# Optimization experiments

Hardware: AMD Instinct MI355X
Metric: run time of the kernel (lower is better)

The kernel has to match this reference:

```python
import jax, jax.numpy as jnp
import numpy as np

B, L, D, H = 2, 1024, 1024, 16
HEAD = D // H
BUCKETS = 256
MAX_REL = 512
ATT_SPAN = BUCKETS          # pos_ebd_size = position_buckets when buckets > 0
SCALE_FACTOR = 3            # 1 (content) + 1 (c2p) + 1 (p2c)


def _log_bucket(rel, bucket_size, max_position):
    """make_log_bucket_position: signed log-bucketed relative positions."""
    sign = jnp.sign(rel).astype(jnp.float32)
    mid = bucket_size // 2
    abs_pos = jnp.where((rel < mid) & (rel > -mid), mid - 1, jnp.abs(rel)).astype(jnp.float32)
    log_pos = jnp.ceil(jnp.log(abs_pos / mid) / np.float32(np.log((max_position - 1) / mid)) * (mid - 1)) + mid
    bucket = jnp.where(abs_pos <= mid, rel.astype(jnp.float32), log_pos * sign)
    return bucket.astype(jnp.int32)


def build_relative_position(q_len, k_len):
    rel = jnp.arange(q_len, dtype=jnp.int32)[:, None] - jnp.arange(k_len, dtype=jnp.int32)[None, :]
    return _log_bucket(rel, BUCKETS, MAX_REL)  # [q_len, k_len]


def setup_inputs() -> dict:
    key = jax.random.key(0)
    ks = jax.random.split(key, 6)
    w = 0.02  # typical init scale, keeps softmax well-conditioned
    return {
        "hidden_states": jax.random.normal(ks[0], (B, L, D), jnp.float32),
        "attention_mask": jnp.ones((B, L), jnp.int32),
        "rel_embeddings": jax.random.normal(ks[1], (2 * ATT_SPAN, D), jnp.float32) * w,
        "Wq": jax.random.normal(ks[2], (D, D), jnp.float32) * w,
        "bq": jnp.zeros((D,), jnp.float32),
        "Wk": jax.random.normal(ks[3], (D, D), jnp.float32) * w,
        "bk": jnp.zeros((D,), jnp.float32),
        "Wv": jax.random.normal(ks[4], (D, D), jnp.float32) * w,
        "bv": jnp.zeros((D,), jnp.float32),
    }


def reference(hidden_states, attention_mask, rel_embeddings, Wq, bq, Wk, bk, Wv, bv):
    Bn, Ln, Dn = hidden_states.shape

    def proj(x, W, b):  # Linear with bias, torch convention y = x W^T + b
        return x @ W.T + b

    def to_heads(x):  # [.., L, D] -> [.., H, L, HEAD]
        return x.reshape(*x.shape[:-1], H, HEAD).swapaxes(-3, -2)

    q = to_heads(proj(hidden_states, Wq, bq))  # [B,H,L,d]
    k = to_heads(proj(hidden_states, Wk, bk))
    v = to_heads(proj(hidden_states, Wv, bv))

    scale = jnp.sqrt(jnp.float32(HEAD * SCALE_FACTOR))
    scores = jnp.einsum('bhqd,bhkd->bhqk', q, k) / scale

    # disentangled relative-position bias (share_att_key=True -> reuse Wq/Wk)
    rel = build_relative_position(Ln, Ln)                     # [L,L] log-bucketed
    pos_k = proj(rel_embeddings, Wk, bk).reshape(2 * ATT_SPAN, H, HEAD)
    pos_q = proj(rel_embeddings, Wq, bq).reshape(2 * ATT_SPAN, H, HEAD)

    # c2p: Q . posK, gathered at (rel + span)
    c2p_att = jnp.einsum('bhqd,phd->bhqp', q, pos_k)          # [B,H,L,2S]
    c2p_idx = jnp.clip(rel + ATT_SPAN, 0, 2 * ATT_SPAN - 1)   # [L,L]
    c2p = jnp.take_along_axis(c2p_att, jnp.broadcast_to(c2p_idx[None, None], (Bn, H, Ln, Ln)), axis=-1)

    # p2c: K . posQ gathered at (-rel + span), then transposed to [q,k]
    p2c_att = jnp.einsum('bhkd,phd->bhkp', k, pos_q)          # [B,H,L,2S]
    p2c_idx = jnp.clip(-rel + ATT_SPAN, 0, 2 * ATT_SPAN - 1)
    p2c = jnp.take_along_axis(p2c_att, jnp.broadcast_to(p2c_idx[None, None], (Bn, H, Ln, Ln)), axis=-1)
    p2c = jnp.swapaxes(p2c, -1, -2)

    scores = scores + (c2p + p2c) / scale

    bias = jnp.where(attention_mask[:, None, None, :] > 0, 0.0, -1e9).astype(scores.dtype)
    probs = jax.nn.softmax(scores + bias, axis=-1)
    ctx = jnp.einsum('bhqk,bhkd->bhqd', probs, v)
    return ctx.swapaxes(1, 2).reshape(Bn, Ln, Dn)
```

## Files before the change

### kernel.cpp

```cpp
#include <hip/hip_runtime.h>


typedef short s8v __attribute__((ext_vector_type(8)));
typedef short s4v __attribute__((ext_vector_type(4)));
typedef float f32x4 __attribute__((ext_vector_type(4)));
typedef float f4v __attribute__((ext_vector_type(4)));

#define QK_SCALE 0.26864243f

__device__ __forceinline__ unsigned short f2bf(float f) {
  unsigned u = __builtin_bit_cast(unsigned, f);
  u += 0x7fffu + ((u >> 16) & 1u);
  return (unsigned short)(u >> 16);
}
__device__ __forceinline__ float bf2f(unsigned short h) {
  unsigned u = ((unsigned)h) << 16;
  return __builtin_bit_cast(float, u);
}

__device__ __forceinline__ void gload_lds16(const void* g, void* l) {
  __builtin_amdgcn_global_load_lds(
      (const __attribute__((address_space(1))) void*)g,
      (__attribute__((address_space(3))) void*)l, 16, 0, 0);
}

__global__ __launch_bounds__(256) void prep_kernel(
    const float* __restrict__ hidden, const float* __restrict__ rel,
    const float* __restrict__ Wq, const float* __restrict__ Wk,
    const float* __restrict__ Wv, const int* __restrict__ mask,
    short* __restrict__ Abf, short* __restrict__ Wbf,
    float* __restrict__ mbias, short* __restrict__ Tt) {
  int idx = blockIdx.x * 256 + threadIdx.x;
  const int NCONV = 1441792;
  if (idx < NCONV) {
    const float* src; short* dst; int off;
    if (idx < 524288) { src = hidden; dst = Abf; off = idx; }
    else if (idx < 655360) { src = rel; dst = Abf + 2048 * 1024; off = idx - 524288; }
    else {
      int j = idx - 655360;
      int w = j / 262144; off = j - w * 262144;
      src = (w == 0) ? Wq : (w == 1) ? Wk : Wv;
      dst = Wbf + w * 1048576;
    }
    f4v v = ((const f4v*)src)[off];
    s4v o;
    o[0] = (short)f2bf(v[0]); o[1] = (short)f2bf(v[1]);
    o[2] = (short)f2bf(v[2]); o[3] = (short)f2bf(v[3]);
    ((s4v*)dst)[off] = o;
  } else {
    int j = idx - NCONV;
    if (j < 2047) {
      int r = j - 1023;
      float fr = (float)r;
      float sign = (r > 0) ? 1.f : ((r < 0) ? -1.f : 0.f);
      float abs_pos = (r < 128 && r > -128) ? 127.f : fabsf(fr);
      const float logc = 1.3843393245589053f;
      float log_pos = ceilf(logf(abs_pos * (1.f / 128.f)) / logc * 127.f) + 128.f;
      float bucket = (abs_pos <= 128.f) ? fr : log_pos * sign;
      int bi = (int)bucket + 256;
      bi = bi < 0 ? 0 : (bi > 511 ? 511 : bi);
      Tt[j] = (short)bi;
    } else if (j < 4095) {
      int m = j - 2047;
      mbias[m] = (mask[m] > 0) ? 0.f : -1e9f;
    }
  }
}

__global__ __launch_bounds__(256) void gemm_qkv(
    const short* __restrict__ Abf, const short* __restrict__ Wbf,
    const float* __restrict__ bq, const float* __restrict__ bk,
    const float* __restrict__ bv,
    short* __restrict__ Qc, short* __restrict__ Kc, short* __restrict__ Vc) {
  __shared__ short As[128 * 64];
  __shared__ short Bs[128 * 64];
  int tid = threadIdx.x;
  int wid = tid >> 6, lane = tid & 63;
  int lr = lane & 15, lg = lane >> 4;
  int wr = wid >> 1, wc = wid & 1;
  int z = blockIdx.z;
  int brow = blockIdx.y * 128;
  if (z == 2 && brow >= 2048) return;
  const short* W = Wbf + z * 1048576;
  const float* bias = (z == 0) ? bq : (z == 1) ? bk : bv;
  short* C = (z == 0) ? Qc : (z == 1) ? Kc : Vc;
  float scale = (z == 2) ? 1.f : QK_SCALE;
  int bcol = blockIdx.x * 128;

  f32x4 acc[4][4];
  for (int i = 0; i < 4; i++)
    for (int j = 0; j < 4; j++) acc[i][j] = (f32x4){0.f, 0.f, 0.f, 0.f};

  for (int k0 = 0; k0 < 1024; k0 += 64) {
    for (int i = 0; i < 4; i++) {
      int n = i * 256 + wid * 64 + lane;
      const short* gA = Abf + (size_t)(brow + (n >> 3)) * 1024 + k0 + (n & 7) * 8;
      gload_lds16(gA, &As[(i * 256 + wid * 64) * 8]);
      const short* gB = W + (size_t)(bcol + (n >> 3)) * 1024 + k0 + (n & 7) * 8;
      gload_lds16(gB, &Bs[(i * 256 + wid * 64) * 8]);
    }
    __syncthreads();
    for (int ks = 0; ks < 2; ks++) {
      s8v af[4], bfv[4];
      for (int mi = 0; mi < 4; mi++)
        af[mi] = *(const s8v*)&As[(wr * 64 + mi * 16 + lr) * 64 + ks * 32 + lg * 8];
      for (int ni = 0; ni < 4; ni++)
        bfv[ni] = *(const s8v*)&Bs[(wc * 64 + ni * 16 + lr) * 64 + ks * 32 + lg * 8];
      for (int mi = 0; mi < 4; mi++)
        for (int ni = 0; ni < 4; ni++)
          acc[mi][ni] = __builtin_amdgcn_mfma_f32_16x16x32_bf16(
              af[mi], bfv[ni], acc[mi][ni], 0, 0, 0);
    }
    __syncthreads();
  }
  for (int mi = 0; mi < 4; mi++)
    for (int ni = 0; ni < 4; ni++) {
      int col = bcol + wc * 64 + ni * 16 + lr;
      float bb = bias[col];
      for (int r = 0; r < 4; r++) {
        int row = brow + wr * 64 + mi * 16 + lg * 4 + r;
        float v = (acc[mi][ni][r] + bb) * scale;
        C[(size_t)row * 1024 + col] = (short)f2bf(v);
      }
    }
}

__global__ __launch_bounds__(256) void pos_gemm(
    const short* __restrict__ Qc, const short* __restrict__ Kc,
    const float* __restrict__ mbias,
    short* __restrict__ c2p, short* __restrict__ p2c) {
  __shared__ short As[128 * 64];
  __shared__ short Bs[128 * 64];
  int tid = threadIdx.x;
  int wid = tid >> 6, lane = tid & 63;
  int lr = lane & 15, lg = lane >> 4;
  int wr = wid >> 1, wc = wid & 1;
  int zz = blockIdx.z;
  int which = zz >> 5;
  int bh = zz & 31;
  int b = bh >> 4, h = bh & 15;
  const short* Arows = (which == 0) ? Qc : Kc;
  const short* Brows = (which == 0) ? Kc : Qc;
  short* Out = (which == 0) ? c2p : p2c;
  int mrow = blockIdx.y * 128;
  int ncol = blockIdx.x * 128;

  for (int i = 0; i < 4; i++) {
    int n = i * 256 + wid * 64 + lane;
    const short* gA = Arows + (size_t)(b * 1024 + mrow + (n >> 3)) * 1024 + h * 64 + (n & 7) * 8;
    gload_lds16(gA, &As[(i * 256 + wid * 64) * 8]);
    const short* gB = Brows + (size_t)(2048 + ncol + (n >> 3)) * 1024 + h * 64 + (n & 7) * 8;
    gload_lds16(gB, &Bs[(i * 256 + wid * 64) * 8]);
  }
  __syncthreads();

  f32x4 acc[4][4];
  for (int i = 0; i < 4; i++)
    for (int j = 0; j < 4; j++) acc[i][j] = (f32x4){0.f, 0.f, 0.f, 0.f};
  for (int ks = 0; ks < 2; ks++) {
    s8v af[4], bfv[4];
    for (int mi = 0; mi < 4; mi++)
      af[mi] = *(const s8v*)&As[(wr * 64 + mi * 16 + lr) * 64 + ks * 32 + lg * 8];
    for (int ni = 0; ni < 4; ni++)
      bfv[ni] = *(const s8v*)&Bs[(wc * 64 + ni * 16 + lr) * 64 + ks * 32 + lg * 8];
    for (int mi = 0; mi < 4; mi++)
      for (int ni = 0; ni < 4; ni++)
        acc[mi][ni] = __builtin_amdgcn_mfma_f32_16x16x32_bf16(
            af[mi], bfv[ni], acc[mi][ni], 0, 0, 0);
  }
  size_t base = (size_t)(b * 16 + h) * 1024;
  for (int mi = 0; mi < 4; mi++)
    for (int ni = 0; ni < 4; ni++)
      for (int r = 0; r < 4; r++) {
        int m = mrow + wr * 64 + mi * 16 + lg * 4 + r;
        int nn = ncol + wc * 64 + ni * 16 + lr;
        float v = acc[mi][ni][r];
        if (which == 1) v += mbias[b * 1024 + m];
        Out[(base + m) * 512 + nn] = (short)f2bf(v);
      }
}

__global__ __launch_bounds__(256) void transpose_v(
    const short* __restrict__ Vc, short* __restrict__ Vt) {
  __shared__ short TL[64 * 72];
  int tid = threadIdx.x;
  int lt = blockIdx.x, h = blockIdx.y, b = blockIdx.z;
  for (int i = 0; i < 2; i++) {
    int n = i * 256 + tid;
    int l = n >> 3, c = n & 7;
    s8v v = *(const s8v*)&Vc[(size_t)(b * 1024 + lt * 64 + l) * 1024 + h * 64 + c * 8];
    *(s8v*)&TL[l * 72 + c * 8] = v;
  }
  __syncthreads();
  for (int i = 0; i < 2; i++) {
    int m = i * 256 + tid;
    int d = m >> 3, c = m & 7;
    s8v o;
    for (int jj = 0; jj < 8; jj++) o[jj] = TL[(c * 8 + jj) * 72 + d];
    *(s8v*)&Vt[((size_t)(b * 16 + h) * 64 + d) * 1024 + lt * 64 + c * 8] = o;
  }
}

template <int NSPLIT>
__global__ __launch_bounds__(256) void attn_kernel(
    const short* __restrict__ Qc, const short* __restrict__ Kc,
    const short* __restrict__ Vt, const short* __restrict__ c2p,
    const short* __restrict__ p2c, const short* __restrict__ Tt,
    float* __restrict__ Opart, float* __restrict__ dpart,
    float* __restrict__ out) {
  const int KSEG = 1024 / NSPLIT;
  const int NT = KSEG / 64;
  const int TLN = 64 + KSEG - 1;
  __shared__ short Kl[64 * 64];
  __shared__ short Vl[64 * 64];
  __shared__ short Pl[4][16 * 72];
  __shared__ short Tl[TLN + 1];
  int tid = threadIdx.x;
  int wid = tid >> 6, lane = tid & 63;
  int lr = lane & 15, lg = lane >> 4;
  int qt = blockIdx.x, h = blockIdx.y, z = blockIdx.z;
  int b = (NSPLIT == 1) ? z : (z >> 2);
  int ks = (NSPLIT == 1) ? 0 : (z & 3);
  int k0seg = ks * KSEG;
  int q0 = qt * 64, qbase = q0 + wid * 16;
  size_t bh1024 = (size_t)(b * 16 + h) * 1024;

  for (int i = tid; i < TLN; i += 256) Tl[i] = Tt[(q0 - k0seg - (KSEG - 1) + 1023) + i];

  s8v aq[2];
  for (int s_ = 0; s_ < 2; s_++)
    aq[s_] = *(const s8v*)&Qc[(size_t)(b * 1024 + qbase + lr) * 1024 + h * 64 + s_ * 32 + lg * 8];

  f32x4 oacc[4];
  for (int n = 0; n < 4; n++) oacc[n] = (f32x4){0.f, 0.f, 0.f, 0.f};
  float dsum[4] = {0.f, 0.f, 0.f, 0.f};
  __syncthreads();

  unsigned short c2g[16], p2g[16];
#pragma unroll
  for (int n = 0; n < 4; n++) {
    int k = k0seg + n * 16 + lr;
    size_t prow = (bh1024 + k) * 512;
    int jb = wid * 16 - lr + (KSEG - 1) - n * 16 + lg * 4;
#pragma unroll
    for (int r = 0; r < 4; r++) {
      int q = qbase + lg * 4 + r;
      int idx = Tl[jb + r];
      c2g[n * 4 + r] = (unsigned short)c2p[(bh1024 + q) * 512 + idx];
      p2g[n * 4 + r] = (unsigned short)p2c[prow + idx];
    }
  }

#pragma unroll
  for (int t = 0; t < NT; ++t) {
    int kt = k0seg + t * 64;
    s8v kvr[2], vvr[2];
#pragma unroll
    for (int i = 0; i < 2; i++) {
      int n = i * 256 + tid;
      int row = n >> 3, cb = n & 7;
      kvr[i] = *(const s8v*)&Kc[(size_t)(b * 1024 + kt + row) * 1024 + h * 64 + cb * 8];
      vvr[i] = *(const s8v*)&Vt[((size_t)(b * 16 + h) * 64 + row) * 1024 + kt + cb * 8];
    }

    unsigned short c2n[16], p2n[16];
    if (t + 1 < NT) {
      int ktl = (t + 1) * 64;
#pragma unroll
      for (int n = 0; n < 4; n++) {
        int k = kt + 64 + n * 16 + lr;
        size_t prow = (bh1024 + k) * 512;
        int jb = wid * 16 - ktl - lr + (KSEG - 1) - n * 16 + lg * 4;
#pragma unroll
        for (int r = 0; r < 4; r++) {
          int q = qbase + lg * 4 + r;
          int idx = Tl[jb + r];
          c2n[n * 4 + r] = (unsigned short)c2p[(bh1024 + q) * 512 + idx];
          p2n[n * 4 + r] = (unsigned short)p2c[prow + idx];
        }
      }
    }

#pragma unroll
    for (int i = 0; i < 2; i++) {
      int n = i * 256 + tid;
      int row = n >> 3, cb = n & 7, cbs = cb ^ (row & 7);
      *(s8v*)&Kl[row * 64 + cbs * 8] = kvr[i];
      *(s8v*)&Vl[row * 64 + cbs * 8] = vvr[i];
    }
    __syncthreads();

    f32x4 sacc[4];
#pragma unroll
    for (int n = 0; n < 4; n++) sacc[n] = (f32x4){0.f, 0.f, 0.f, 0.f};
#pragma unroll
    for (int s_ = 0; s_ < 2; s_++)
#pragma unroll
      for (int n = 0; n < 4; n++) {
        int row = n * 16 + lr, cb = s_ * 4 + lg, cbs = cb ^ (row & 7);
        s8v bk_ = *(const s8v*)&Kl[row * 64 + cbs * 8];
        sacc[n] = __builtin_amdgcn_mfma_f32_16x16x32_bf16(aq[s_], bk_, sacc[n], 0, 0, 0);
      }

#pragma unroll
    for (int n = 0; n < 4; n++)
#pragma unroll
      for (int r = 0; r < 4; r++) {
        float bias = bf2f(c2g[n * 4 + r]) + bf2f(p2g[n * 4 + r]);
        float p = __expf(sacc[n][r] + bias);
        dsum[r] += p;
        Pl[wid][(lg * 4 + r) * 72 + n * 16 + lr] = (short)f2bf(p);
      }
    __syncthreads();

#pragma unroll
    for (int s_ = 0; s_ < 2; s_++) {
      s8v ap = *(const s8v*)&Pl[wid][lr * 72 + s_ * 32 + lg * 8];
#pragma unroll
      for (int n = 0; n < 4; n++) {
        int row = n * 16 + lr, cb = s_ * 4 + lg, cbs = cb ^ (row & 7);
        s8v bv_ = *(const s8v*)&Vl[row * 64 + cbs * 8];
        oacc[n] = __builtin_amdgcn_mfma_f32_16x16x32_bf16(ap, bv_, oacc[n], 0, 0, 0);
      }
    }
    __syncthreads();

    if (t + 1 < NT) {
#pragma unroll
      for (int i = 0; i < 16; i++) { c2g[i] = c2n[i]; p2g[i] = p2n[i]; }
    }
  }

  for (int m = 1; m < 16; m <<= 1)
    for (int r = 0; r < 4; r++) dsum[r] += __shfl_xor(dsum[r], m, 64);

  if (NSPLIT == 1) {
    for (int n = 0; n < 4; n++)
      for (int r = 0; r < 4; r++) {
        int q = qbase + lg * 4 + r;
        int d = n * 16 + lr;
        out[(size_t)(b * 1024 + q) * 1024 + h * 64 + d] = oacc[n][r] / dsum[r];
      }
  } else {
    size_t po = ((size_t)(z * 16 + h)) * 65536;
    for (int n = 0; n < 4; n++)
      for (int r = 0; r < 4; r++) {
        int q = qbase + lg * 4 + r;
        Opart[po + (size_t)q * 64 + n * 16 + lr] = oacc[n][r];
      }
    if (lr == 0)
      for (int r = 0; r < 4; r++)
        dpart[(z * 16 + h) * 1024 + qbase + lg * 4 + r] = dsum[r];
  }
}

__global__ __launch_bounds__(256) void combine_kernel(
    const float* __restrict__ Opart, const float* __restrict__ dpart,
    float* __restrict__ out) {
  int idx = blockIdx.x * 256 + threadIdx.x;
  int pos = idx * 4;
  int b = pos >> 20;
  int q = (pos >> 10) & 1023;
  int hd = pos & 1023;
  int h = hd >> 6, d = hd & 63;
  f4v s = (f4v){0.f, 0.f, 0.f, 0.f};
  float dn = 0.f;
  for (int ks = 0; ks < 4; ks++) {
    int zh = (b * 4 + ks) * 16 + h;
    s += *(const f4v*)&Opart[(size_t)zh * 65536 + q * 64 + d];
    dn += dpart[zh * 1024 + q];
  }
  f4v r = s / dn;
  *(f4v*)&out[pos] = r;
}

extern "C" void kernel_launch(void* const* d_in, const int* in_sizes, int n_in,
                              void* d_out, int out_size, void* d_ws, size_t ws_size,
                              hipStream_t stream) {
  (void)in_sizes; (void)n_in; (void)out_size;
  const float* hidden = (const float*)d_in[0];
  const int* mask = (const int*)d_in[1];
  const float* rel = (const float*)d_in[2];
  const float* Wq = (const float*)d_in[3];
  const float* bq = (const float*)d_in[4];
  const float* Wk = (const float*)d_in[5];
  const float* bk = (const float*)d_in[6];
  const float* Wv = (const float*)d_in[7];
  const float* bv = (const float*)d_in[8];
  float* out = (float*)d_out;

  char* w = (char*)d_ws;
  short* Abf = (short*)w; w += 2560 * 1024 * 2;
  short* Wbf = (short*)w; w += 3 * 1024 * 1024 * 2;
  short* Qc  = (short*)w; w += 2560 * 1024 * 2;
  short* Kc  = (short*)w; w += 2560 * 1024 * 2;
  short* Vc  = (short*)w; w += 2560 * 1024 * 2;
  short* Vt  = (short*)w; w += 2 * 16 * 64 * 1024 * 2;
  short* c2p = (short*)w; w += (size_t)2 * 16 * 1024 * 512 * 2;
  short* p2c = (short*)w; w += (size_t)2 * 16 * 1024 * 512 * 2;
  short* Tt  = (short*)w; w += 4096;
  float* mbias = (float*)w; w += 8192;
  float* Opart = (float*)w; w += (size_t)8 * 16 * 1024 * 64 * 4;
  float* dpart = (float*)w; w += 8 * 16 * 1024 * 4;
  size_t need = (size_t)(w - (char*)d_ws);

  prep_kernel<<<5648, 256, 0, stream>>>(hidden, rel, Wq, Wk, Wv, mask, Abf, Wbf, mbias, Tt);
  gemm_qkv<<<dim3(8, 20, 3), 256, 0, stream>>>(Abf, Wbf, bq, bk, bv, Qc, Kc, Vc);
  pos_gemm<<<dim3(4, 8, 64), 256, 0, stream>>>(Qc, Kc, mbias, c2p, p2c);
  transpose_v<<<dim3(16, 16, 2), 256, 0, stream>>>(Vc, Vt);
  if (ws_size >= need) {
    attn_kernel<4><<<dim3(16, 16, 8), 256, 0, stream>>>(Qc, Kc, Vt, c2p, p2c, Tt,
                                                        Opart, dpart, out);
    combine_kernel<<<2048, 256, 0, stream>>>(Opart, dpart, out);
  } else {
    attn_kernel<1><<<dim3(16, 16, 2), 256, 0, stream>>>(Qc, Kc, Vt, c2p, p2c, Tt,
                                                        Opart, dpart, out);
  }
}
```

Baseline: 157.6 us.

## Double-buffer K/V tiles with async global-to-LDS loads and drop a barrier

The attention kernel now double-buffers the K and V tiles in LDS and fills them with direct global-to-LDS loads. It issues the next tile's loads before computing on the current one, so the register round-trip and the stall at the top of each iteration go away. The barrier between the P store and the P·V MFMA becomes a wave-local lgkmcnt wait, since each wave reads only its own Pl slice. The cost is doubled LDS for K and V, and correctness now depends on the async-load completion and swizzle addressing being right; there is no explicit vmcnt wait before the next tile is used.

```diff
diff --git a/kernel.cpp b/kernel.cpp
--- a/kernel.cpp
+++ b/kernel.cpp
@@ -211,8 +211,8 @@
   const int KSEG = 1024 / NSPLIT;
   const int NT = KSEG / 64;
   const int TLN = 64 + KSEG - 1;
-  __shared__ short Kl[64 * 64];
-  __shared__ short Vl[64 * 64];
+  __shared__ short Kl[2][64 * 64];
+  __shared__ short Vl[2][64 * 64];
   __shared__ short Pl[4][16 * 72];
   __shared__ short Tl[TLN + 1];
   int tid = threadIdx.x;
@@ -236,59 +236,46 @@
   float dsum[4] = {0.f, 0.f, 0.f, 0.f};
   __syncthreads();
 
-  unsigned short c2g[16], p2g[16];
-#pragma unroll
-  for (int n = 0; n < 4; n++) {
-    int k = k0seg + n * 16 + lr;
-    size_t prow = (bh1024 + k) * 512;
-    int jb = wid * 16 - lr + (KSEG - 1) - n * 16 + lg * 4;
-#pragma unroll
-    for (int r = 0; r < 4; r++) {
-      int q = qbase + lg * 4 + r;
-      int idx = Tl[jb + r];
-      c2g[n * 4 + r] = (unsigned short)c2p[(bh1024 + q) * 512 + idx];
-      p2g[n * 4 + r] = (unsigned short)p2c[prow + idx];
-    }
-  }
-
-#pragma unroll
-  for (int t = 0; t < NT; ++t) {
-    int kt = k0seg + t * 64;
-    s8v kvr[2], vvr[2];
+  auto stage = [&](int t, int buf) {
 #pragma unroll
     for (int i = 0; i < 2; i++) {
       int n = i * 256 + tid;
-      int row = n >> 3, cb = n & 7;
-      kvr[i] = *(const s8v*)&Kc[(size_t)(b * 1024 + kt + row) * 1024 + h * 64 + cb * 8];
-      vvr[i] = *(const s8v*)&Vt[((size_t)(b * 16 + h) * 64 + row) * 1024 + kt + cb * 8];
-    }
-
-    unsigned short c2n[16], p2n[16];
+      int row = n >> 3, cswz = n & 7, cb = cswz ^ (row & 7);
+      gload_lds16(&Kc[(size_t)(b * 1024 + k0seg + t * 64 + row) * 1024 + h * 64 + cb * 8],
+                  &Kl[buf][(i * 256 + wid * 64) * 8]);
+      gload_lds16(&Vt[((size_t)(b * 16 + h) * 64 + row) * 1024 + k0seg + t * 64 + cb * 8],
+                  &Vl[buf][(i * 256 + wid * 64) * 8]);
+    }
+  };
+  auto gather = [&](int t, unsigned short* cg, unsigned short* pg) {
+#pragma unroll
+    for (int n = 0; n < 4; n++) {
+      int k = k0seg + t * 64 + n * 16 + lr;
+      size_t prow = (bh1024 + k) * 512;
+      int jb = wid * 16 - t * 64 - lr + (KSEG - 1) - n * 16 + lg * 4;
+#pragma unroll
+      for (int r = 0; r < 4; r++) {
+        int q = qbase + lg * 4 + r;
+        int idx = Tl[jb + r];
+        cg[n * 4 + r] = (unsigned short)c2p[(bh1024 + q) * 512 + idx];
+        pg[n * 4 + r] = (unsigned short)p2c[prow + idx];
+      }
+    }
+  };
+
+  unsigned short c2g[16], p2g[16], c2n[16], p2n[16];
+  stage(0, 0);
+  gather(0, c2g, p2g);
+  __syncthreads();
+
+#pragma unroll
+  for (int t = 0; t < NT; ++t) {
+    const int cur = t & 1, nxt = cur ^ 1;
+
     if (t + 1 < NT) {
-      int ktl = (t + 1) * 64;
-#pragma unroll
-      for (int n = 0; n < 4; n++) {
-        int k = kt + 64 + n * 16 + lr;
-        size_t prow = (bh1024 + k) * 512;
-        int jb = wid * 16 - ktl - lr + (KSEG - 1) - n * 16 + lg * 4;
-#pragma unroll
-        for (int r = 0; r < 4; r++) {
-          int q = qbase + lg * 4 + r;
-          int idx = Tl[jb + r];
-          c2n[n * 4 + r] = (unsigned short)c2p[(bh1024 + q) * 512 + idx];
-          p2n[n * 4 + r] = (unsigned short)p2c[prow + idx];
-        }
-      }
-    }
-
-#pragma unroll
-    for (int i = 0; i < 2; i++) {
-      int n = i * 256 + tid;
-      int row = n >> 3, cb = n & 7, cbs = cb ^ (row & 7);
-      *(s8v*)&Kl[row * 64 + cbs * 8] = kvr[i];
-      *(s8v*)&Vl[row * 64 + cbs * 8] = vvr[i];
-    }
-    __syncthreads();
+      stage(t + 1, nxt);
+      gather(t + 1, c2n, p2n);
+    }
 
     f32x4 sacc[4];
 #pragma unroll
@@ -298,7 +285,7 @@
 #pragma unroll
       for (int n = 0; n < 4; n++) {
         int row = n * 16 + lr, cb = s_ * 4 + lg, cbs = cb ^ (row & 7);
-        s8v bk_ = *(const s8v*)&Kl[row * 64 + cbs * 8];
+        s8v bk_ = *(const s8v*)&Kl[cur][row * 64 + cbs * 8];
         sacc[n] = __builtin_amdgcn_mfma_f32_16x16x32_bf16(aq[s_], bk_, sacc[n], 0, 0, 0);
       }
 
@@ -311,7 +298,7 @@
         dsum[r] += p;
         Pl[wid][(lg * 4 + r) * 72 + n * 16 + lr] = (short)f2bf(p);
       }
-    __syncthreads();
+    asm volatile("s_waitcnt lgkmcnt(0)" ::: "memory");
 
 #pragma unroll
     for (int s_ = 0; s_ < 2; s_++) {
@@ -319,10 +306,11 @@
 #pragma unroll
       for (int n = 0; n < 4; n++) {
         int row = n * 16 + lr, cb = s_ * 4 + lg, cbs = cb ^ (row & 7);
-        s8v bv_ = *(const s8v*)&Vl[row * 64 + cbs * 8];
+        s8v bv_ = *(const s8v*)&Vl[cur][row * 64 + cbs * 8];
         oacc[n] = __builtin_amdgcn_mfma_f32_16x16x32_bf16(ap, bv_, oacc[n], 0, 0, 0);
       }
     }
+
     __syncthreads();
 
     if (t + 1 < NT) {
```

Result: no change. 155.6 us (-1.3%).
